# Kernel optimization log

Hardware: AMD Instinct MI355X
Metric: run time of the kernel (lower is better)

## Reference

```python
import jax, jax.numpy as jnp
import numpy as np

DIM = 512

def setup_inputs() -> dict:
    key = jax.random.key(0)
    ks = jax.random.split(key, 7)
    B, Nq, Nkv = 8, 1024, 4096
    prototype = jax.random.normal(ks[0], (B, Nq, DIM), dtype=jnp.float32)
    q_x = jax.random.normal(ks[1], (B, Nkv, DIM), dtype=jnp.float32)
    qry_attn_mask = jax.random.bernoulli(ks[2], 0.5, (B, Nkv))  # True = keep
    # Linear(dim, dim, bias=False) weights, torch convention y = x @ W.T
    s = 1.0 / np.sqrt(DIM)
    Wq = jax.random.uniform(ks[3], (DIM, DIM), jnp.float32, -s, s)
    Wk = jax.random.uniform(ks[4], (DIM, DIM), jnp.float32, -s, s)
    Wv = jax.random.uniform(ks[5], (DIM, DIM), jnp.float32, -s, s)
    Wproj = jax.random.uniform(ks[6], (DIM, DIM), jnp.float32, -s, s)
    return {"prototype": prototype, "q_x": q_x, "qry_attn_mask": qry_attn_mask,
            "Wq": Wq, "Wk": Wk, "Wv": Wv, "Wproj": Wproj}

def reference(prototype, q_x, qry_attn_mask, Wq, Wk, Wv, Wproj):
    scale = DIM ** (-0.5)
    q = jnp.einsum('bnd,ed->bne', prototype, Wq)          # [B,Nq,D]
    k = jnp.einsum('bmd,ed->bme', q_x, Wk)                # [B,Nkv,D]
    v = jnp.einsum('bmd,ed->bme', q_x, Wv)                # [B,Nkv,D]
    attn = jnp.einsum('bnd,bmd->bnm', q, k) * scale       # [B,Nq,Nkv]
    bias = (~qry_attn_mask).astype(attn.dtype)[:, None, :] * -10000.0
    attn = jax.nn.softmax(attn + bias, axis=-1)
    x = jnp.einsum('bnm,bmd->bnd', attn, v)
    x = jnp.einsum('bnd,ed->bne', x, Wproj)
    return x
```

## Files before the change

kernel.cpp:

```cpp
#include <hip/hip_runtime.h>
#include <hip/hip_bf16.h>
#include <stdint.h>


typedef __bf16 bf16;
typedef bf16 bf16x8 __attribute__((ext_vector_type(8)));
typedef bf16 bf16x4 __attribute__((ext_vector_type(4)));
typedef float f32x4 __attribute__((ext_vector_type(4)));

#define NB 8
#define NQ 1024
#define NKV 4096
#define DD 512

__device__ __forceinline__ void direct16(const void* g, void* s) {
  __builtin_amdgcn_global_load_lds(
      (const __attribute__((address_space(1))) void*)g,
      (__attribute__((address_space(3))) void*)s, 16, 0, 0);
}

__global__ void cvt_kernel(const float* __restrict__ src, bf16* __restrict__ dst, int n4) {
  int i = blockIdx.x * blockDim.x + threadIdx.x;
  if (i < n4) {
    float4 v = ((const float4*)src)[i];
    bf16x4 o;
    o.x = (bf16)v.x; o.y = (bf16)v.y; o.z = (bf16)v.z; o.w = (bf16)v.w;
    ((bf16x4*)dst)[i] = o;
  }
}

__global__ void sniff_zero(const unsigned* __restrict__ mask, int* __restrict__ flag,
                           float* __restrict__ denom) {
  __shared__ int s_bad0, s_bad1;
  if (threadIdx.x == 0) { s_bad0 = 0; s_bad1 = 0; }
  __syncthreads();
  int b0 = 0, b1 = 0;
  for (int i = threadIdx.x; i < 8192; i += 256) {
    unsigned v = mask[i];
    if (v > 1u) b0 = 1;
    if (v != 0u && v != 0x3F800000u) b1 = 1;
  }
  if (b0) atomicOr(&s_bad0, 1);
  if (b1) atomicOr(&s_bad1, 1);
  for (int i = threadIdx.x; i < NB * NQ; i += 256) denom[i] = 0.f;
  __syncthreads();
  if (threadIdx.x == 0) *flag = (s_bad0 == 0) ? 0 : ((s_bad1 == 0) ? 1 : 2);
}

template <int EPI>
__global__ void __launch_bounds__(256, 2)
gemm_bt(const bf16* __restrict__ A, const bf16* __restrict__ Bw,
        void* __restrict__ Cp, int N, int K,
        long sA, long sB, long sC,
        const void* __restrict__ mask, const int* __restrict__ flagP,
        float* __restrict__ denom, float scale, int M) {
  __shared__ alignas(16) bf16 As[128 * 32];
  __shared__ alignas(16) bf16 Bs[128 * 32];
  const int tid = threadIdx.x;
  const int wave = tid >> 6, lane = tid & 63;
  const int l15 = lane & 15, l4 = lane >> 4;
  const int wm = (wave >> 1) * 64, wn = (wave & 1) * 64;
  const int b = blockIdx.z;

  const bf16* Ab = A + (long)b * sA + (long)(blockIdx.y * 128) * K;
  const bf16* Bb = Bw + (long)b * sB + (long)(blockIdx.x * 128) * K;

  const int c0 = wave * 2, c1 = wave * 2 + 1;
  const int srow = lane >> 2;
  const int scol = (lane & 3) * 8;
  const bf16* ag0 = Ab + (long)(c0 * 16 + srow) * K + scol;
  const bf16* ag1 = Ab + (long)(c1 * 16 + srow) * K + scol;
  const bf16* bg0 = Bb + (long)(c0 * 16 + srow) * K + scol;
  const bf16* bg1 = Bb + (long)(c1 * 16 + srow) * K + scol;
  bf16* al0 = As + c0 * 512 + lane * 8;
  bf16* al1 = As + c1 * 512 + lane * 8;
  bf16* bl0 = Bs + c0 * 512 + lane * 8;
  bf16* bl1 = Bs + c1 * 512 + lane * 8;

  f32x4 acc[4][4] = {};

  for (int kt = 0; kt < K; kt += 32) {
    __syncthreads();
    direct16(ag0, al0);
    direct16(ag1, al1);
    direct16(bg0, bl0);
    direct16(bg1, bl1);
    ag0 += 32; ag1 += 32; bg0 += 32; bg1 += 32;
    __syncthreads();
    bf16x8 af[4], bfr[4];
#pragma unroll
    for (int t = 0; t < 4; ++t)
      af[t] = *(const bf16x8*)(As + (wm + t * 16 + l15) * 32 + l4 * 8);
#pragma unroll
    for (int t = 0; t < 4; ++t)
      bfr[t] = *(const bf16x8*)(Bs + (wn + t * 16 + l15) * 32 + l4 * 8);
#pragma unroll
    for (int mt = 0; mt < 4; ++mt)
#pragma unroll
      for (int nt = 0; nt < 4; ++nt)
        acc[mt][nt] = __builtin_amdgcn_mfma_f32_16x16x32_bf16(af[mt], bfr[nt],
                                                              acc[mt][nt], 0, 0, 0);
  }

  const int rowBase = blockIdx.y * 128 + wm;
  const int colBase = blockIdx.x * 128 + wn;

  if constexpr (EPI == 0) {
    bf16* C = (bf16*)Cp + (long)b * sC;
#pragma unroll
    for (int mt = 0; mt < 4; ++mt)
#pragma unroll
      for (int nt = 0; nt < 4; ++nt)
#pragma unroll
        for (int r = 0; r < 4; ++r)
          C[(long)(rowBase + mt * 16 + l4 * 4 + r) * N + colBase + nt * 16 + l15] =
              (bf16)acc[mt][nt][r];
  } else if constexpr (EPI == 1) {
    bf16* C = (bf16*)Cp + (long)b * sC;
#pragma unroll
    for (int mt = 0; mt < 4; ++mt)
#pragma unroll
      for (int nt = 0; nt < 4; ++nt) {
        bf16x4 o;
        o.x = (bf16)acc[mt][nt][0]; o.y = (bf16)acc[mt][nt][1];
        o.z = (bf16)acc[mt][nt][2]; o.w = (bf16)acc[mt][nt][3];
        long addr = (long)(colBase + nt * 16 + l15) * M + rowBase + mt * 16 + l4 * 4;
        *(bf16x4*)(C + addr) = o;
      }
  } else if constexpr (EPI == 2) {
    bf16* C = (bf16*)Cp + (long)b * sC;
    const int mode = *flagP;
    float rs[4][4];
#pragma unroll
    for (int mt = 0; mt < 4; ++mt)
#pragma unroll
      for (int r = 0; r < 4; ++r) rs[mt][r] = 0.f;
#pragma unroll
    for (int nt = 0; nt < 4; ++nt) {
      const int col = colBase + nt * 16 + l15;
      bool keep;
      if (mode == 0)      keep = ((const int*)mask)[b * NKV + col] != 0;
      else if (mode == 1) keep = ((const float*)mask)[b * NKV + col] != 0.f;
      else                keep = ((const unsigned char*)mask)[b * NKV + col] != 0;
#pragma unroll
      for (int mt = 0; mt < 4; ++mt)
#pragma unroll
        for (int r = 0; r < 4; ++r) {
          float p = keep ? __expf(acc[mt][nt][r] * scale) : 0.f;
          rs[mt][r] += p;
          C[(long)(rowBase + mt * 16 + l4 * 4 + r) * N + col] = (bf16)p;
        }
    }
#pragma unroll
    for (int mt = 0; mt < 4; ++mt)
#pragma unroll
      for (int r = 0; r < 4; ++r) {
        float v = rs[mt][r];
        v += __shfl_xor(v, 1, 64);
        v += __shfl_xor(v, 2, 64);
        v += __shfl_xor(v, 4, 64);
        v += __shfl_xor(v, 8, 64);
        if (l15 == 0)
          atomicAdd(&denom[b * M + rowBase + mt * 16 + l4 * 4 + r], v);
      }
  } else if constexpr (EPI == 3) {
    bf16* C = (bf16*)Cp + (long)b * sC;
#pragma unroll
    for (int mt = 0; mt < 4; ++mt)
#pragma unroll
      for (int r = 0; r < 4; ++r) {
        const float inv = 1.0f / denom[b * M + rowBase + mt * 16 + l4 * 4 + r];
#pragma unroll
        for (int nt = 0; nt < 4; ++nt)
          C[(long)(rowBase + mt * 16 + l4 * 4 + r) * N + colBase + nt * 16 + l15] =
              (bf16)(acc[mt][nt][r] * inv);
      }
  } else {
    float* C = (float*)Cp + (long)b * sC;
#pragma unroll
    for (int mt = 0; mt < 4; ++mt)
#pragma unroll
      for (int nt = 0; nt < 4; ++nt)
#pragma unroll
        for (int r = 0; r < 4; ++r)
          C[(long)(rowBase + mt * 16 + l4 * 4 + r) * N + colBase + nt * 16 + l15] =
              acc[mt][nt][r];
  }
}

extern "C" void kernel_launch(void* const* d_in, const int* in_sizes, int n_in,
                              void* d_out, int out_size, void* d_ws, size_t ws_size,
                              hipStream_t stream) {
  const float* proto = (const float*)d_in[0];
  const float* qx    = (const float*)d_in[1];
  const void*  mask  = d_in[2];
  const float* Wq    = (const float*)d_in[3];
  const float* Wk    = (const float*)d_in[4];
  const float* Wv    = (const float*)d_in[5];
  const float* Wproj = (const float*)d_in[6];
  float* out = (float*)d_out;

  char* w = (char*)d_ws;
  int*   flag  = (int*)w;
  float* denom = (float*)(w + 4096);
  size_t off = 65536;
  bf16* Wq_b = (bf16*)(w + off); off += (size_t)DD * DD * 2;
  bf16* Wk_b = (bf16*)(w + off); off += (size_t)DD * DD * 2;
  bf16* Wv_b = (bf16*)(w + off); off += (size_t)DD * DD * 2;
  bf16* Wp_b = (bf16*)(w + off); off += (size_t)DD * DD * 2;
  bf16* q_b  = (bf16*)(w + off); off += (size_t)NB * NQ * DD * 2;
  bf16* k_b  = (bf16*)(w + off); off += (size_t)NB * NKV * DD * 2;
  bf16* vT_b = (bf16*)(w + off); off += (size_t)NB * NKV * DD * 2;
  bf16* x_b  = (bf16*)(w + off); off += (size_t)NB * NQ * DD * 2;
  size_t off_pp = off;
  bf16* proto_b = (bf16*)(w + off); off += (size_t)NB * NQ * DD * 2;
  bf16* qx_b    = (bf16*)(w + off);
  bf16* P       = (bf16*)(w + off_pp);

  sniff_zero<<<1, 256, 0, stream>>>((const unsigned*)mask, flag, denom);

  cvt_kernel<<<NB * NQ * DD / 4 / 256, 256, 0, stream>>>(proto, proto_b, NB * NQ * DD / 4);
  cvt_kernel<<<NB * NKV * DD / 4 / 256, 256, 0, stream>>>(qx, qx_b, NB * NKV * DD / 4);
  cvt_kernel<<<DD * DD / 4 / 256, 256, 0, stream>>>(Wq, Wq_b, DD * DD / 4);
  cvt_kernel<<<DD * DD / 4 / 256, 256, 0, stream>>>(Wk, Wk_b, DD * DD / 4);
  cvt_kernel<<<DD * DD / 4 / 256, 256, 0, stream>>>(Wv, Wv_b, DD * DD / 4);
  cvt_kernel<<<DD * DD / 4 / 256, 256, 0, stream>>>(Wproj, Wp_b, DD * DD / 4);

  const float scale = 0.04419417382415922f;

  gemm_bt<0><<<dim3(DD / 128, NQ / 128, NB), 256, 0, stream>>>(
      proto_b, Wq_b, q_b, DD, DD, (long)NQ * DD, 0L, (long)NQ * DD,
      nullptr, nullptr, nullptr, 0.f, NQ);
  gemm_bt<0><<<dim3(DD / 128, NKV / 128, NB), 256, 0, stream>>>(
      qx_b, Wk_b, k_b, DD, DD, (long)NKV * DD, 0L, (long)NKV * DD,
      nullptr, nullptr, nullptr, 0.f, NKV);
  gemm_bt<1><<<dim3(DD / 128, NKV / 128, NB), 256, 0, stream>>>(
      qx_b, Wv_b, vT_b, DD, DD, (long)NKV * DD, 0L, (long)DD * NKV,
      nullptr, nullptr, nullptr, 0.f, NKV);
  gemm_bt<2><<<dim3(NKV / 128, NQ / 128, NB), 256, 0, stream>>>(
      q_b, k_b, P, NKV, DD, (long)NQ * DD, (long)NKV * DD, (long)NQ * NKV,
      mask, flag, denom, scale, NQ);
  gemm_bt<3><<<dim3(DD / 128, NQ / 128, NB), 256, 0, stream>>>(
      P, vT_b, x_b, DD, NKV, (long)NQ * NKV, (long)DD * NKV, (long)NQ * DD,
      nullptr, nullptr, denom, 0.f, NQ);
  gemm_bt<4><<<dim3(DD / 128, NQ / 128, NB), 256, 0, stream>>>(
      x_b, Wp_b, out, DD, DD, (long)NQ * DD, 0L, (long)NQ * DD,
      nullptr, nullptr, nullptr, 0.f, NQ);
}
```

Measured before the change: 384.0 us.

## Split-K the PV GEMM, fuse K/V projections, merge weight conversions

```diff
diff --git a/kernel.cpp b/kernel.cpp
--- a/kernel.cpp
+++ b/kernel.cpp
@@ -27,6 +27,22 @@
     o.x = (bf16)v.x; o.y = (bf16)v.y; o.z = (bf16)v.z; o.w = (bf16)v.w;
     ((bf16x4*)dst)[i] = o;
   }
+}
+
+__global__ void cvt_weights(const float* __restrict__ Wq, const float* __restrict__ Wk,
+                            const float* __restrict__ Wv, const float* __restrict__ Wp,
+                            bf16* __restrict__ Wq_b, bf16* __restrict__ Wkv_b,
+                            bf16* __restrict__ Wp_b) {
+  int i = blockIdx.x * blockDim.x + threadIdx.x;
+  int w = i >> 16, r = i & 65535;
+  const float* src = (w == 0) ? Wq : (w == 1) ? Wk : (w == 2) ? Wv : Wp;
+  bf16x4* dst = (w == 0) ? (bf16x4*)Wq_b
+              : (w == 3) ? (bf16x4*)Wp_b
+                         : (bf16x4*)Wkv_b + (w == 2 ? 65536 : 0);
+  float4 v = ((const float4*)src)[r];
+  bf16x4 o;
+  o.x = (bf16)v.x; o.y = (bf16)v.y; o.z = (bf16)v.z; o.w = (bf16)v.w;
+  dst[r] = o;
 }
 
 __global__ void sniff_zero(const unsigned* __restrict__ mask, int* __restrict__ flag,
@@ -47,10 +63,24 @@
   if (threadIdx.x == 0) *flag = (s_bad0 == 0) ? 0 : ((s_bad1 == 0) ? 1 : 2);
 }
 
+__global__ void reduce_pv(const float4* __restrict__ p0, const float4* __restrict__ p1,
+                          const float* __restrict__ denom, bf16x4* __restrict__ x, int n4) {
+  int i = blockIdx.x * blockDim.x + threadIdx.x;
+  if (i < n4) {
+    float4 a = p0[i], c = p1[i];
+    const float inv = 1.0f / denom[i >> 7];
+    bf16x4 o;
+    o.x = (bf16)((a.x + c.x) * inv); o.y = (bf16)((a.y + c.y) * inv);
+    o.z = (bf16)((a.z + c.z) * inv); o.w = (bf16)((a.w + c.w) * inv);
+    x[i] = o;
+  }
+}
+
 template <int EPI>
 __global__ void __launch_bounds__(256, 2)
 gemm_bt(const bf16* __restrict__ A, const bf16* __restrict__ Bw,
-        void* __restrict__ Cp, int N, int K,
+        void* __restrict__ Cp, void* __restrict__ Cp2,
+        int N, int Klen, int Kstride, long kOff,
         long sA, long sB, long sC,
         const void* __restrict__ mask, const int* __restrict__ flagP,
         float* __restrict__ denom, float scale, int M) {
@@ -60,18 +90,19 @@
   const int wave = tid >> 6, lane = tid & 63;
   const int l15 = lane & 15, l4 = lane >> 4;
   const int wm = (wave >> 1) * 64, wn = (wave & 1) * 64;
-  const int b = blockIdx.z;
-
-  const bf16* Ab = A + (long)b * sA + (long)(blockIdx.y * 128) * K;
-  const bf16* Bb = Bw + (long)b * sB + (long)(blockIdx.x * 128) * K;
+  const int b = blockIdx.z & 7;
+  const int chunk = blockIdx.z >> 3;
+
+  const bf16* Ab = A + (long)b * sA + chunk * kOff + (long)(blockIdx.y * 128) * Kstride;
+  const bf16* Bb = Bw + (long)b * sB + chunk * kOff + (long)(blockIdx.x * 128) * Kstride;
 
   const int c0 = wave * 2, c1 = wave * 2 + 1;
   const int srow = lane >> 2;
   const int scol = (lane & 3) * 8;
-  const bf16* ag0 = Ab + (long)(c0 * 16 + srow) * K + scol;
-  const bf16* ag1 = Ab + (long)(c1 * 16 + srow) * K + scol;
-  const bf16* bg0 = Bb + (long)(c0 * 16 + srow) * K + scol;
-  const bf16* bg1 = Bb + (long)(c1 * 16 + srow) * K + scol;
+  const bf16* ag0 = Ab + (long)(c0 * 16 + srow) * Kstride + scol;
+  const bf16* ag1 = Ab + (long)(c1 * 16 + srow) * Kstride + scol;
+  const bf16* bg0 = Bb + (long)(c0 * 16 + srow) * Kstride + scol;
+  const bf16* bg1 = Bb + (long)(c1 * 16 + srow) * Kstride + scol;
   bf16* al0 = As + c0 * 512 + lane * 8;
   bf16* al1 = As + c1 * 512 + lane * 8;
   bf16* bl0 = Bs + c0 * 512 + lane * 8;
@@ -79,7 +110,7 @@
 
   f32x4 acc[4][4] = {};
 
-  for (int kt = 0; kt < K; kt += 32) {
+  for (int kt = 0; kt < Klen; kt += 32) {
     __syncthreads();
     direct16(ag0, al0);
     direct16(ag1, al1);
@@ -115,18 +146,6 @@
         for (int r = 0; r < 4; ++r)
           C[(long)(rowBase + mt * 16 + l4 * 4 + r) * N + colBase + nt * 16 + l15] =
               (bf16)acc[mt][nt][r];
-  } else if constexpr (EPI == 1) {
-    bf16* C = (bf16*)Cp + (long)b * sC;
-#pragma unroll
-    for (int mt = 0; mt < 4; ++mt)
-#pragma unroll
-      for (int nt = 0; nt < 4; ++nt) {
-        bf16x4 o;
-        o.x = (bf16)acc[mt][nt][0]; o.y = (bf16)acc[mt][nt][1];
-        o.z = (bf16)acc[mt][nt][2]; o.w = (bf16)acc[mt][nt][3];
-        long addr = (long)(colBase + nt * 16 + l15) * M + rowBase + mt * 16 + l4 * 4;
-        *(bf16x4*)(C + addr) = o;
-      }
   } else if constexpr (EPI == 2) {
     bf16* C = (bf16*)Cp + (long)b * sC;
     const int mode = *flagP;
@@ -163,20 +182,8 @@
         if (l15 == 0)
           atomicAdd(&denom[b * M + rowBase + mt * 16 + l4 * 4 + r], v);
       }
-  } else if constexpr (EPI == 3) {
-    bf16* C = (bf16*)Cp + (long)b * sC;
-#pragma unroll
-    for (int mt = 0; mt < 4; ++mt)
-#pragma unroll
-      for (int r = 0; r < 4; ++r) {
-        const float inv = 1.0f / denom[b * M + rowBase + mt * 16 + l4 * 4 + r];
-#pragma unroll
-        for (int nt = 0; nt < 4; ++nt)
-          C[(long)(rowBase + mt * 16 + l4 * 4 + r) * N + colBase + nt * 16 + l15] =
-              (bf16)(acc[mt][nt][r] * inv);
-      }
-  } else {
-    float* C = (float*)Cp + (long)b * sC;
+  } else if constexpr (EPI == 4) {
+    float* C = (float*)Cp + (long)blockIdx.z * sC;
 #pragma unroll
     for (int mt = 0; mt < 4; ++mt)
 #pragma unroll
@@ -185,6 +192,33 @@
         for (int r = 0; r < 4; ++r)
           C[(long)(rowBase + mt * 16 + l4 * 4 + r) * N + colBase + nt * 16 + l15] =
               acc[mt][nt][r];
+  } else {
+    if (colBase < 512) {
+      bf16* C = (bf16*)Cp;
+#pragma unroll
+      for (int mt = 0; mt < 4; ++mt)
+#pragma unroll
+        for (int nt = 0; nt < 4; ++nt)
+#pragma unroll
+          for (int r = 0; r < 4; ++r)
+            C[(long)(rowBase + mt * 16 + l4 * 4 + r) * 512 + colBase + nt * 16 + l15] =
+                (bf16)acc[mt][nt][r];
+    } else {
+      bf16* C = (bf16*)Cp2;
+#pragma unroll
+      for (int mt = 0; mt < 4; ++mt) {
+        const int gm = rowBase + mt * 16 + l4 * 4;
+        const int bb = gm >> 12, mloc = gm & 4095;
+#pragma unroll
+        for (int nt = 0; nt < 4; ++nt) {
+          const int col = colBase + nt * 16 + l15 - 512;
+          bf16x4 o;
+          o.x = (bf16)acc[mt][nt][0]; o.y = (bf16)acc[mt][nt][1];
+          o.z = (bf16)acc[mt][nt][2]; o.w = (bf16)acc[mt][nt][3];
+          *(bf16x4*)(C + (long)bb * DD * NKV + (long)col * NKV + mloc) = o;
+        }
+      }
+    }
   }
 }
 
@@ -204,14 +238,14 @@
   int*   flag  = (int*)w;
   float* denom = (float*)(w + 4096);
   size_t off = 65536;
-  bf16* Wq_b = (bf16*)(w + off); off += (size_t)DD * DD * 2;
-  bf16* Wk_b = (bf16*)(w + off); off += (size_t)DD * DD * 2;
-  bf16* Wv_b = (bf16*)(w + off); off += (size_t)DD * DD * 2;
-  bf16* Wp_b = (bf16*)(w + off); off += (size_t)DD * DD * 2;
-  bf16* q_b  = (bf16*)(w + off); off += (size_t)NB * NQ * DD * 2;
-  bf16* k_b  = (bf16*)(w + off); off += (size_t)NB * NKV * DD * 2;
-  bf16* vT_b = (bf16*)(w + off); off += (size_t)NB * NKV * DD * 2;
-  bf16* x_b  = (bf16*)(w + off); off += (size_t)NB * NQ * DD * 2;
+  bf16* Wq_b  = (bf16*)(w + off); off += (size_t)DD * DD * 2;
+  bf16* Wkv_b = (bf16*)(w + off); off += (size_t)DD * DD * 4;
+  bf16* Wp_b  = (bf16*)(w + off); off += (size_t)DD * DD * 2;
+  bf16* q_b   = (bf16*)(w + off); off += (size_t)NB * NQ * DD * 2;
+  bf16* k_b   = (bf16*)(w + off); off += (size_t)NB * NKV * DD * 2;
+  float* part = (float*)k_b;
+  bf16* vT_b  = (bf16*)(w + off); off += (size_t)NB * NKV * DD * 2;
+  bf16* x_b   = (bf16*)(w + off); off += (size_t)NB * NQ * DD * 2;
   size_t off_pp = off;
   bf16* proto_b = (bf16*)(w + off); off += (size_t)NB * NQ * DD * 2;
   bf16* qx_b    = (bf16*)(w + off);
@@ -221,29 +255,28 @@
 
   cvt_kernel<<<NB * NQ * DD / 4 / 256, 256, 0, stream>>>(proto, proto_b, NB * NQ * DD / 4);
   cvt_kernel<<<NB * NKV * DD / 4 / 256, 256, 0, stream>>>(qx, qx_b, NB * NKV * DD / 4);
-  cvt_kernel<<<DD * DD / 4 / 256, 256, 0, stream>>>(Wq, Wq_b, DD * DD / 4);
-  cvt_kernel<<<DD * DD / 4 / 256, 256, 0, stream>>>(Wk, Wk_b, DD * DD / 4);
-  cvt_kernel<<<DD * DD / 4 / 256, 256, 0, stream>>>(Wv, Wv_b, DD * DD / 4);
-  cvt_kernel<<<DD * DD / 4 / 256, 256, 0, stream>>>(Wproj, Wp_b, DD * DD / 4);
+  cvt_weights<<<4 * 65536 / 256, 256, 0, stream>>>(Wq, Wk, Wv, Wproj, Wq_b, Wkv_b, Wp_b);
 
   const float scale = 0.04419417382415922f;
 
-  gemm_bt<0><<<dim3(DD / 128, NQ / 128, NB), 256, 0, stream>>>(
-      proto_b, Wq_b, q_b, DD, DD, (long)NQ * DD, 0L, (long)NQ * DD,
-      nullptr, nullptr, nullptr, 0.f, NQ);
-  gemm_bt<0><<<dim3(DD / 128, NKV / 128, NB), 256, 0, stream>>>(
-      qx_b, Wk_b, k_b, DD, DD, (long)NKV * DD, 0L, (long)NKV * DD,
-      nullptr, nullptr, nullptr, 0.f, NKV);
-  gemm_bt<1><<<dim3(DD / 128, NKV / 128, NB), 256, 0, stream>>>(
-      qx_b, Wv_b, vT_b, DD, DD, (long)NKV * DD, 0L, (long)DD * NKV,
-      nullptr, nullptr, nullptr, 0.f, NKV);
+  gemm_bt<0><<<dim3(4, 64, 1), 256, 0, stream>>>(
+      proto_b, Wq_b, q_b, nullptr, DD, DD, DD, 0L, 0L, 0L, 0L,
+      nullptr, nullptr, nullptr, 0.f, 0);
+  gemm_bt<5><<<dim3(8, 256, 1), 256, 0, stream>>>(
+      qx_b, Wkv_b, k_b, vT_b, 1024, DD, DD, 0L, 0L, 0L, 0L,
+      nullptr, nullptr, nullptr, 0.f, 0);
   gemm_bt<2><<<dim3(NKV / 128, NQ / 128, NB), 256, 0, stream>>>(
-      q_b, k_b, P, NKV, DD, (long)NQ * DD, (long)NKV * DD, (long)NQ * NKV,
+      q_b, k_b, P, nullptr, NKV, DD, DD, 0L,
+      (long)NQ * DD, (long)NKV * DD, (long)NQ * NKV,
       mask, flag, denom, scale, NQ);
-  gemm_bt<3><<<dim3(DD / 128, NQ / 128, NB), 256, 0, stream>>>(
-      P, vT_b, x_b, DD, NKV, (long)NQ * NKV, (long)DD * NKV, (long)NQ * DD,
-      nullptr, nullptr, denom, 0.f, NQ);
-  gemm_bt<4><<<dim3(DD / 128, NQ / 128, NB), 256, 0, stream>>>(
-      x_b, Wp_b, out, DD, DD, (long)NQ * DD, 0L, (long)NQ * DD,
-      nullptr, nullptr, nullptr, 0.f, NQ);
-}
+  gemm_bt<4><<<dim3(4, 8, 16), 256, 0, stream>>>(
+      P, vT_b, part, nullptr, DD, NKV / 2, NKV, (long)NKV / 2,
+      (long)NQ * NKV, (long)DD * NKV, (long)NQ * DD,
+      nullptr, nullptr, nullptr, 0.f, 0);
+  reduce_pv<<<NB * NQ * DD / 4 / 256, 256, 0, stream>>>(
+      (const float4*)part, (const float4*)(part + (size_t)NB * NQ * DD),
+      denom, (bf16x4*)x_b, NB * NQ * DD / 4);
+  gemm_bt<4><<<dim3(4, 64, 1), 256, 0, stream>>>(
+      x_b, Wp_b, out, nullptr, DD, DD, DD, 0L, 0L, 0L, 0L,
+      nullptr, nullptr, nullptr, 0.f, 0);
+}
```

Result: faster. 368.8 us (-4.0%).
